# Kernel tuning notes

Measured on AMD Instinct MI355X. Metric: run time of the kernel, lower is better.

The kernel has to match this reference:

```python
import jax, jax.numpy as jnp
import numpy as np

B, T, D, H = 2, 2048, 1024, 16
HD = D // H  # 64


def _rotary_tables(t, hd):
    # standard RoPE cos/sin tables, shape [T, hd]
    inv_freq = 1.0 / (10000.0 ** (jnp.arange(0, hd, 2, dtype=jnp.float32) / hd))
    freqs = jnp.arange(t, dtype=jnp.float32)[:, None] * inv_freq[None, :]  # [T, hd/2]
    emb = jnp.concatenate([freqs, freqs], axis=-1)  # [T, hd]
    return jnp.cos(emb), jnp.sin(emb)


def setup_inputs() -> dict:
    key = jax.random.key(0)
    kx, kq, kk, kv, kp = jax.random.split(key, 5)
    x = jax.random.normal(kx, (B, T, D), dtype=jnp.float32)
    cos_t, sin_t = _rotary_tables(T, HD)
    cos = jnp.broadcast_to(cos_t[None], (B, T, HD)).astype(jnp.float32)
    sin = jnp.broadcast_to(sin_t[None], (B, T, HD)).astype(jnp.float32)
    scale = 0.02
    Wq = jax.random.normal(kq, (D, D), dtype=jnp.float32) * scale
    Wk = jax.random.normal(kk, (D, D), dtype=jnp.float32) * scale
    Wv = jax.random.normal(kv, (D, D), dtype=jnp.float32) * scale
    Wp = jax.random.normal(kp, (D, D), dtype=jnp.float32) * scale
    return {"x": x, "cos": cos, "sin": sin, "Wq": Wq, "Wk": Wk, "Wv": Wv, "Wp": Wp}


def _rotate_half(x):
    x1, x2 = jnp.split(x, 2, axis=-1)
    return jnp.concatenate([-x2, x1], axis=-1)


def reference(x, cos, sin, Wq, Wk, Wv, Wp):
    b, t, d = x.shape
    h, hd = H, HD
    # torch Linear: y = x @ W.T
    q = jnp.einsum('btd,ed->bte', x, Wq).reshape(b, t, h, hd)
    k = jnp.einsum('btd,ed->bte', x, Wk).reshape(b, t, h, hd)
    v = jnp.einsum('btd,ed->bte', x, Wv).reshape(b, t, h, hd)
    # RoPE, cos/sin [B,T,hd] -> broadcast over heads (unsqueeze_dim=2)
    c = cos[:, :, None, :]
    s = sin[:, :, None, :]
    q = q * c + _rotate_half(q) * s
    k = k * c + _rotate_half(k) * s
    # causal attention, softmax scale = 1/sqrt(head_dim) (flash_attn default)
    scale = 1.0 / np.sqrt(hd).astype(np.float32)
    scores = jnp.einsum('bqhd,bkhd->bhqk', q, k) * scale  # [B,H,T,T]
    mask = jnp.tril(jnp.ones((t, t), dtype=bool))
    scores = jnp.where(mask[None, None], scores, jnp.finfo(scores.dtype).min)
    probs = jax.nn.softmax(scores, axis=-1)
    out = jnp.einsum('bhqk,bkhd->bqhd', probs, v).reshape(b, t, d)
    return jnp.einsum('btd,ed->bte', out, Wp)
```

## Files before the change

### kernel.cpp

```cpp
#include <hip/hip_runtime.h>
#include <hip/hip_bf16.h>

typedef __attribute__((ext_vector_type(8))) short bf16x8s;
typedef __attribute__((ext_vector_type(4))) float f32x4;
typedef __attribute__((ext_vector_type(16))) float f32x16;
typedef __attribute__((ext_vector_type(4))) __bf16 bf16x4;
typedef __attribute__((ext_vector_type(8))) __bf16 bf16x8;

typedef const __attribute__((address_space(1))) void gvoid_t;
typedef __attribute__((address_space(3))) void lvoid_t;

constexpr int Bc = 2, Tc = 2048, Dc = 1024, Hc = 16, HDc = 64;
constexpr int Mc = Bc * Tc;

__global__ void cvt_all(const float* __restrict__ x,
                        const float* __restrict__ wq, const float* __restrict__ wk,
                        const float* __restrict__ wv, const float* __restrict__ wp,
                        __bf16* __restrict__ xb, __bf16* __restrict__ wb) {
  const int bid = blockIdx.x;
  const float* src;
  __bf16* dst;
  int i;
  if (bid < 4096) {
    src = x; dst = xb; i = (bid * 256 + threadIdx.x) * 4;
  } else {
    const int r = bid - 4096;
    const int w = r >> 10;
    src = (w == 0) ? wq : (w == 1) ? wk : (w == 2) ? wv : wp;
    dst = wb + (size_t)w * (Dc * Dc);
    i = ((r & 1023) * 256 + threadIdx.x) * 4;
  }
  float4 v = *(const float4*)(src + i);
  bf16x4 o;
  o[0] = (__bf16)v.x; o[1] = (__bf16)v.y; o[2] = (__bf16)v.z; o[3] = (__bf16)v.w;
  *(bf16x4*)(dst + i) = o;
}

__launch_bounds__(512, 2)
__global__ void gemm_qkv(const __bf16* __restrict__ A,
                         const __bf16* __restrict__ W,
                         __bf16* __restrict__ outb,
                         __bf16* __restrict__ vtout,
                         const float* __restrict__ cbt,
                         const float* __restrict__ sbt) {
  __shared__ __bf16 Albuf[2][128 * 64];
  __shared__ __bf16 Bbuf[2][3][128 * 64];
  const int tid = threadIdx.x;
  const int lane = tid & 63, wid = tid >> 6;
  const int wr = wid >> 1, wc = wid & 1;
  const int lr = lane & 15, lg = lane >> 4;
  const int lid = blockIdx.x + 8 * blockIdx.y;
  const int xcd = lid & 7, g = lid >> 3;
  const int brow = (xcd * 4 + (g & 3)) * 128;
  const int bcol = (g >> 2) * 128;

  f32x4 acc[3][2][4] = {};

  const char* Ag = (const char*)(A + (size_t)brow * Dc);
  const char* Bg = (const char*)(W + (size_t)bcol * Dc);
  const int r0s = tid >> 3;
  const int scol = (((tid & 7) ^ (r0s & 7)) << 4);
  const int lr7 = lr & 7;

#define STAGE(K0, BUF)                                                                    \
  do {                                                                                    \
    _Pragma("unroll")                                                                     \
    for (int i_ = 0; i_ < 2; ++i_) {                                                      \
      __builtin_amdgcn_global_load_lds(                                                   \
          (gvoid_t*)(Ag + (size_t)(i_ * 64 + r0s) * (Dc * 2) + (K0)*2 + scol),            \
          (lvoid_t*)((char*)Albuf[BUF] + i_ * 8192 + wid * 1024), 16, 0, 0);              \
      _Pragma("unroll")                                                                   \
      for (int z_ = 0; z_ < 3; ++z_)                                                      \
        __builtin_amdgcn_global_load_lds(                                                 \
            (gvoid_t*)(Bg + (size_t)z_ * (Dc * Dc * 2) +                                  \
                       (size_t)(i_ * 64 + r0s) * (Dc * 2) + (K0)*2 + scol),               \
            (lvoid_t*)((char*)Bbuf[BUF][z_] + i_ * 8192 + wid * 1024), 16, 0, 0);         \
    }                                                                                     \
  } while (0)

  STAGE(0, 0);
  asm volatile("s_waitcnt vmcnt(0)" ::: "memory");
  __builtin_amdgcn_sched_barrier(0);
  __builtin_amdgcn_s_barrier();
  __builtin_amdgcn_sched_barrier(0);

  for (int s = 0; s < 16; ++s) {
    if (s + 1 < 16) STAGE((s + 1) * 64, (s + 1) & 1);
    __builtin_amdgcn_sched_barrier(0);
    const char* Al = (const char*)Albuf[s & 1];
    const char* Bl0 = (const char*)Bbuf[s & 1][0];
#pragma unroll
    for (int kk = 0; kk < 2; ++kk) {
      const int sw = ((kk * 4 + lg) ^ lr7) << 4;
      bf16x8s af[2];
#pragma unroll
      for (int m = 0; m < 2; ++m)
        af[m] = *(const bf16x8s*)(Al + (wr * 32 + m * 16 + lr) * 128 + sw);
#pragma unroll
      for (int z = 0; z < 3; ++z) {
        const char* Bl = Bl0 + z * (128 * 64 * 2);
        bf16x8s bfv[4];
#pragma unroll
        for (int n = 0; n < 4; ++n)
          bfv[n] = *(const bf16x8s*)(Bl + (wc * 64 + n * 16 + lr) * 128 + sw);
        __builtin_amdgcn_s_setprio(1);
#pragma unroll
        for (int m = 0; m < 2; ++m)
#pragma unroll
          for (int n = 0; n < 4; ++n)
            acc[z][m][n] =
                __builtin_amdgcn_mfma_f32_16x16x32_bf16(af[m], bfv[n], acc[z][m][n], 0, 0, 0);
        __builtin_amdgcn_s_setprio(0);
      }
    }
    asm volatile("s_waitcnt vmcnt(0)" ::: "memory");
    __builtin_amdgcn_sched_barrier(0);
    __builtin_amdgcn_s_barrier();
    __builtin_amdgcn_sched_barrier(0);
  }
#undef STAGE

  const int h = (bcol >> 6) + wc;
#pragma unroll
  for (int z = 0; z < 2; ++z) {
    const float scl = (z == 0) ? 0.18033688011112042f : 1.0f;
    __bf16* dst = outb + (size_t)z * ((size_t)Mc * Dc);
#pragma unroll
    for (int m = 0; m < 2; ++m) {
#pragma unroll
      for (int j = 0; j < 4; ++j) {
        const int gm = brow + wr * 32 + m * 16 + lg * 4 + j;
        const int bb = gm >> 11, t = gm & (Tc - 1);
        const float* cbase = cbt + (size_t)gm * HDc;
        const float* sbase = sbt + (size_t)gm * HDc;
#pragma unroll
        for (int n = 0; n < 2; ++n) {
          const int i = n * 16 + lr;
          const float c0 = cbase[i], s0 = sbase[i];
          const float v0 = acc[z][m][n][j], v1 = acc[z][m][n + 2][j];
          acc[z][m][n][j]     = (v0 * c0 - v1 * s0) * scl;
          acc[z][m][n + 2][j] = (v1 * c0 + v0 * s0) * scl;
        }
        __bf16* rowp = dst + (((size_t)bb * Hc + h) * Tc + t) * HDc;
#pragma unroll
        for (int n = 0; n < 4; ++n) rowp[n * 16 + lr] = (__bf16)acc[z][m][n][j];
      }
    }
  }

  {
    const int bb2 = brow >> 11, t0b = brow & (Tc - 1);
    __bf16* tile_t = (__bf16*)Albuf;
#pragma unroll
    for (int h2 = 0; h2 < 2; ++h2) {
      __syncthreads();
      if (wc == h2) {
#pragma unroll
        for (int n = 0; n < 4; ++n)
#pragma unroll
          for (int m = 0; m < 2; ++m)
#pragma unroll
            for (int j = 0; j < 4; ++j)
              tile_t[(n * 16 + lr) * 136 + wr * 32 + m * 16 + lg * 4 + j] =
                  (__bf16)acc[2][m][n][j];
      }
      __syncthreads();
      const int hh2 = (bcol >> 6) + h2;
#pragma unroll
      for (int p = 0; p < 2; ++p) {
        const int r = p * 32 + (tid >> 4);
        const int c8 = (tid & 15) * 8;
        bf16x8 vvv = *(const bf16x8*)(tile_t + r * 136 + c8);
        *(bf16x8*)(vtout + (((size_t)bb2 * Hc + hh2) * HDc + r) * Tc + t0b + c8) = vvv;
      }
    }
  }
}

__launch_bounds__(256, 2)
__global__ void gemm_proj(const __bf16* __restrict__ A, const __bf16* __restrict__ W,
                          float* __restrict__ outf) {
  __shared__ __bf16 Alds[128 * 64];
  __shared__ __bf16 Blds[64 * 64];
  const int tid = threadIdx.x;
  const int lane = tid & 63, wid = tid >> 6;
  const int lr = lane & 15, lg = lane >> 4;
  const int lid = blockIdx.x + (int)gridDim.x * blockIdx.y;
  const int xcd = lid & 7, g = lid >> 3;
  const int brow = (xcd * 4 + (g & 3)) * 128;
  const int bcol = (g >> 2) * 64;
  f32x4 acc[2][4] = {};
  const char* Ag = (const char*)(A + (size_t)brow * Dc);
  const char* Bg = (const char*)(W + (size_t)bcol * Dc);
  const int r0 = tid >> 3;
  const int cb = (tid & 7) * 16;
  for (int k0 = 0; k0 < Dc; k0 += 64) {
#pragma unroll
    for (int i = 0; i < 4; ++i) {
      const int r = i * 32 + r0;
      const int ldsoff = (i * 256 + wid * 64) * 16;
      __builtin_amdgcn_global_load_lds(
          (gvoid_t*)(Ag + (size_t)r * (Dc * 2) + k0 * 2 + cb),
          (lvoid_t*)((char*)Alds + ldsoff), 16, 0, 0);
    }
#pragma unroll
    for (int i = 0; i < 2; ++i) {
      const int r = i * 32 + r0;
      const int ldsoff = (i * 256 + wid * 64) * 16;
      __builtin_amdgcn_global_load_lds(
          (gvoid_t*)(Bg + (size_t)r * (Dc * 2) + k0 * 2 + cb),
          (lvoid_t*)((char*)Blds + ldsoff), 16, 0, 0);
    }
    __syncthreads();
#pragma unroll
    for (int kk = 0; kk < 2; ++kk) {
      const int col = kk * 32 + lg * 8;
      bf16x8s af[2], bfv[4];
#pragma unroll
      for (int m = 0; m < 2; ++m)
        af[m] = *(const bf16x8s*)(Alds + (wid * 32 + m * 16 + lr) * 64 + col);
#pragma unroll
      for (int n = 0; n < 4; ++n)
        bfv[n] = *(const bf16x8s*)(Blds + (n * 16 + lr) * 64 + col);
#pragma unroll
      for (int m = 0; m < 2; ++m)
#pragma unroll
        for (int n = 0; n < 4; ++n)
          acc[m][n] = __builtin_amdgcn_mfma_f32_16x16x32_bf16(bfv[n], af[m], acc[m][n], 0, 0, 0);
    }
    __syncthreads();
  }
#pragma unroll
  for (int m = 0; m < 2; ++m) {
    const int gm = brow + wid * 32 + m * 16 + lr;
    float* rowp = outf + (size_t)gm * Dc + bcol;
#pragma unroll
    for (int n = 0; n < 4; ++n) {
      float4 fv;
      fv.x = acc[m][n][0]; fv.y = acc[m][n][1]; fv.z = acc[m][n][2]; fv.w = acc[m][n][3];
      *(float4*)(rowp + n * 16 + lg * 4) = fv;
    }
  }
}

__launch_bounds__(512, 4)
__global__ void attn_kernel(const __bf16* __restrict__ Q, const __bf16* __restrict__ K,
                            const __bf16* __restrict__ Vt, __bf16* __restrict__ O) {
  __shared__ __bf16 Klds[2][128 * 64];
  __shared__ __bf16 Vlds[2][64 * 128];
  const int f = blockIdx.x;
  const int xcd = f & 7, g = f >> 3;
  const int pass = g >> 4, g4 = g & 15;
  const int bh = xcd * 4 + pass;
  const int qt = ((pass >> 1) & 1) ? (15 - g4) : g4;
  const int tid = threadIdx.x;
  const int lane = tid & 63, wid = tid >> 6;
  const int qq = wid >> 1, kp = wid & 1;
  const int q31 = lane & 31, hh = lane >> 5;
  const int k3 = q31 & 7;
  const int v15 = q31 & 15;
  const __bf16* Qp = Q + (size_t)bh * Tc * HDc;
  const char* Kb = (const char*)(K + (size_t)bh * Tc * HDc);
  const char* Vb = (const char*)(Vt + (size_t)bh * HDc * Tc);

  const int units = qt + 1;

  const int sr = tid >> 3;
  const int sxor = ((tid & 7) ^ (sr & 7)) << 4;
  const int vr = tid >> 4;
  const int vxor = ((tid & 15) ^ (vr & 15)) << 4;
  const char* vsrc = Vb + (size_t)vr * (Tc * 2) + vxor;

  const int q0w = qt * 128 + qq * 32;
  bf16x8s qf[4];
#pragma unroll
  for (int ks = 0; ks < 4; ++ks)
    qf[ks] = *(const bf16x8s*)(Qp + (q0w + q31) * HDc + ks * 16 + hh * 8);

  const int b = bh >> 4, h = bh & 15;

  f32x16 acc0 = {}, acc1 = {};
  float lsum = 0.f;

#define STAGE(IT, BUF)                                                                   \
  do {                                                                                   \
    _Pragma("unroll")                                                                    \
    for (int i_ = 0; i_ < 2; ++i_) {                                                     \
      __builtin_amdgcn_global_load_lds(                                                  \
          (gvoid_t*)(Kb + (size_t)((IT) * 128 + i_ * 64 + sr) * 128 + sxor),             \
          (lvoid_t*)((char*)Klds[BUF] + i_ * 8192 + wid * 1024), 16, 0, 0);              \
      __builtin_amdgcn_global_load_lds(                                                  \
          (gvoid_t*)(vsrc + (size_t)i_ * 32 * (Tc * 2) + (IT) * 256),                    \
          (lvoid_t*)((char*)Vlds[BUF] + i_ * 8192 + wid * 1024), 16, 0, 0);              \
    }                                                                                    \
  } while (0)

  STAGE(0, 0);
  asm volatile("s_waitcnt vmcnt(0)" ::: "memory");
  __builtin_amdgcn_sched_barrier(0);
  __builtin_amdgcn_s_barrier();
  __builtin_amdgcn_sched_barrier(0);

  for (int u = 0; u < units; ++u) {
    if (u + 1 < units) STAGE(u + 1, (u + 1) & 1);
    __builtin_amdgcn_sched_barrier(0);

    const bool last = (u == qt);
    if (!(last && kp == 1 && qq < 2)) {
      const char* Kl = (const char*)Klds[u & 1];
      const char* Vl = (const char*)Vlds[u & 1];
      const bool fin = last && ((qq >> 1) == kp);
      const int thr = q0w + q31 - u * 128 - kp * 64 - 4 * hh;

#pragma unroll
      for (int ct = 0; ct < 2; ++ct) {
        bf16x8s kf[4];
#pragma unroll
        for (int ks = 0; ks < 4; ++ks)
          kf[ks] = *(const bf16x8s*)(Kl + (kp * 64 + ct * 32 + q31) * 128 +
                                     (((2 * ks + hh) ^ k3) << 4));
        f32x16 z = {};
        __builtin_amdgcn_s_setprio(1);
#pragma unroll
        for (int ks = 0; ks < 4; ++ks)
          z = __builtin_amdgcn_mfma_f32_32x32x16_bf16(kf[ks], qf[ks], z, 0, 0, 0);
        __builtin_amdgcn_s_setprio(0);

        unsigned w0[4], w1[4];
#pragma unroll
        for (int n = 0; n < 4; ++n) {
          float e[4];
#pragma unroll
          for (int j = 0; j < 4; ++j) {
            float ev = __builtin_amdgcn_exp2f(z[n * 4 + j]);
            if (fin && (ct * 32 + n * 8 + j > thr)) ev = 0.f;
            lsum += ev;
            e[j] = ev;
          }
          asm("v_cvt_pk_bf16_f32 %0, %1, %2" : "=v"(w0[n]) : "v"(e[0]), "v"(e[1]));
          asm("v_cvt_pk_bf16_f32 %0, %1, %2" : "=v"(w1[n]) : "v"(e[2]), "v"(e[3]));
        }

        bf16x8s pfr[2];
#pragma unroll
        for (int ks2 = 0; ks2 < 2; ++ks2) {
          unsigned a = w0[2 * ks2], bb2 = w0[2 * ks2 + 1];
          unsigned c = w1[2 * ks2], d = w1[2 * ks2 + 1];
          asm volatile("v_permlane32_swap_b32 %0, %1" : "+v"(a), "+v"(bb2));
          asm volatile("v_permlane32_swap_b32 %0, %1" : "+v"(c), "+v"(d));
          union { unsigned u[4]; bf16x8s v; } uu;
          uu.u[0] = a; uu.u[1] = c; uu.u[2] = bb2; uu.u[3] = d;
          pfr[ks2] = uu.v;
        }

        __builtin_amdgcn_s_setprio(1);
#pragma unroll
        for (int ks2 = 0; ks2 < 2; ++ks2) {
          const int so = ((kp * 8 + ct * 4 + 2 * ks2 + hh) ^ v15) << 4;
          const bf16x8s va0 = *(const bf16x8s*)(Vl + q31 * 256 + so);
          const bf16x8s va1 = *(const bf16x8s*)(Vl + (32 + q31) * 256 + so);
          acc0 = __builtin_amdgcn_mfma_f32_32x32x16_bf16(va0, pfr[ks2], acc0, 0, 0, 0);
          acc1 = __builtin_amdgcn_mfma_f32_32x32x16_bf16(va1, pfr[ks2], acc1, 0, 0, 0);
        }
        __builtin_amdgcn_s_setprio(0);
      }
    }

    if (u + 1 < units) {
      asm volatile("s_waitcnt vmcnt(0)" ::: "memory");
      __builtin_amdgcn_sched_barrier(0);
      __builtin_amdgcn_s_barrier();
      __builtin_amdgcn_sched_barrier(0);
    }
  }
#undef STAGE

  __syncthreads();
  float* kscr = (float*)&Klds[0][0];
  float* lscr = (float*)&Vlds[0][0];
  if (kp == 1) {
#pragma unroll
    for (int i = 0; i < 16; ++i) {
      kscr[qq * 2048 + i * 64 + lane] = acc0[i];
      kscr[qq * 2048 + 1024 + i * 64 + lane] = acc1[i];
    }
    lscr[qq * 64 + lane] = lsum;
  }
  __syncthreads();
  if (kp == 0) {
#pragma unroll
    for (int i = 0; i < 16; ++i) {
      acc0[i] += kscr[qq * 2048 + i * 64 + lane];
      acc1[i] += kscr[qq * 2048 + 1024 + i * 64 + lane];
    }
    lsum += lscr[qq * 64 + lane];
    const float lt = lsum + __shfl_xor(lsum, 32);
    const float linv = 1.f / lt;
    const int t = q0w + q31;
    __bf16* dst = O + ((size_t)b * Tc + t) * Dc + h * HDc;
#pragma unroll
    for (int qd = 0; qd < 4; ++qd) {
      bf16x4 o0, o1;
#pragma unroll
      for (int j = 0; j < 4; ++j) {
        o0[j] = (__bf16)(acc0[qd * 4 + j] * linv);
        o1[j] = (__bf16)(acc1[qd * 4 + j] * linv);
      }
      *(bf16x4*)(dst + qd * 8 + hh * 4) = o0;
      *(bf16x4*)(dst + 32 + qd * 8 + hh * 4) = o1;
    }
  }
}

extern "C" void kernel_launch(void* const* d_in, const int* in_sizes, int n_in,
                              void* d_out, int out_size, void* d_ws, size_t ws_size,
                              hipStream_t stream) {
  const float* x   = (const float*)d_in[0];
  const float* cbt = (const float*)d_in[1];
  const float* sbt = (const float*)d_in[2];
  const float* Wq  = (const float*)d_in[3];
  const float* Wk  = (const float*)d_in[4];
  const float* Wv  = (const float*)d_in[5];
  const float* Wp  = (const float*)d_in[6];
  float* out = (float*)d_out;
  char* ws = (char*)d_ws;
  __bf16* xb = (__bf16*)(ws);
  __bf16* wb = (__bf16*)(ws + (8u << 20));
  __bf16* qb = (__bf16*)(ws + (16u << 20));
  __bf16* vt = (__bf16*)(ws + (40u << 20));
  __bf16* ao = (__bf16*)(ws + (48u << 20));
  __bf16* kb = qb + (size_t)Mc * Dc;

  cvt_all<<<8192, 256, 0, stream>>>(x, Wq, Wk, Wv, Wp, xb, wb);
  gemm_qkv<<<dim3(8, 32), 512, 0, stream>>>(xb, wb, qb, vt, cbt, sbt);
  attn_kernel<<<512, 512, 0, stream>>>(qb, kb, vt, ao);
  gemm_proj<<<dim3(16, 32), 256, 0, stream>>>(ao, wb + 3u * (Dc * Dc), out);
}
```

Measured before the change: 95.52 us.

## Switch QKV GEMM to 4-stage K=32 pipeline with partial vmcnt waits

The QKV projection GEMM moves from a double-buffered K=64 loop to a four-buffer K=32 ring with two stages in flight, waiting only on the older loads via vmcnt counts instead of draining all loads each iteration. The LDS layout changes to pack two 32-wide rows per 128-byte line with a new XOR swizzle, and the fragment load addressing is updated to match. This is meant to hide global load latency better. In exchange it doubles the number of barriers and iterations, and the staging math must stay consistent with the swizzle.

```diff
diff --git a/kernel.cpp b/kernel.cpp
--- a/kernel.cpp
+++ b/kernel.cpp
@@ -43,8 +43,8 @@
                          __bf16* __restrict__ vtout,
                          const float* __restrict__ cbt,
                          const float* __restrict__ sbt) {
-  __shared__ __bf16 Albuf[2][128 * 64];
-  __shared__ __bf16 Bbuf[2][3][128 * 64];
+  __shared__ __bf16 Abuf[4][128 * 32];
+  __shared__ __bf16 Bbuf[4][3][128 * 32];
   const int tid = threadIdx.x;
   const int lane = tid & 63, wid = tid >> 6;
   const int wr = wid >> 1, wc = wid & 1;
@@ -58,65 +58,65 @@
 
   const char* Ag = (const char*)(A + (size_t)brow * Dc);
   const char* Bg = (const char*)(W + (size_t)bcol * Dc);
-  const int r0s = tid >> 3;
-  const int scol = (((tid & 7) ^ (r0s & 7)) << 4);
-  const int lr7 = lr & 7;
+  const int rp = tid >> 3;
+  const int unswz = (tid & 7) ^ (rp & 7);
+  const int srow = 2 * rp + (unswz >> 2);
+  const int skoff = (unswz & 3) * 16;
 
 #define STAGE(K0, BUF)                                                                    \
   do {                                                                                    \
+    __builtin_amdgcn_global_load_lds(                                                     \
+        (gvoid_t*)(Ag + (size_t)srow * (Dc * 2) + (K0)*2 + skoff),                        \
+        (lvoid_t*)((char*)Abuf[BUF] + tid * 16), 16, 0, 0);                               \
     _Pragma("unroll")                                                                     \
-    for (int i_ = 0; i_ < 2; ++i_) {                                                      \
+    for (int z_ = 0; z_ < 3; ++z_)                                                        \
       __builtin_amdgcn_global_load_lds(                                                   \
-          (gvoid_t*)(Ag + (size_t)(i_ * 64 + r0s) * (Dc * 2) + (K0)*2 + scol),            \
-          (lvoid_t*)((char*)Albuf[BUF] + i_ * 8192 + wid * 1024), 16, 0, 0);              \
-      _Pragma("unroll")                                                                   \
-      for (int z_ = 0; z_ < 3; ++z_)                                                      \
-        __builtin_amdgcn_global_load_lds(                                                 \
-            (gvoid_t*)(Bg + (size_t)z_ * (Dc * Dc * 2) +                                  \
-                       (size_t)(i_ * 64 + r0s) * (Dc * 2) + (K0)*2 + scol),               \
-            (lvoid_t*)((char*)Bbuf[BUF][z_] + i_ * 8192 + wid * 1024), 16, 0, 0);         \
-    }                                                                                     \
+          (gvoid_t*)(Bg + (size_t)z_ * (Dc * Dc * 2) + (size_t)srow * (Dc * 2) +          \
+                     (K0)*2 + skoff),                                                     \
+          (lvoid_t*)((char*)Bbuf[BUF][z_] + tid * 16), 16, 0, 0);                         \
   } while (0)
 
   STAGE(0, 0);
-  asm volatile("s_waitcnt vmcnt(0)" ::: "memory");
-  __builtin_amdgcn_sched_barrier(0);
-  __builtin_amdgcn_s_barrier();
-  __builtin_amdgcn_sched_barrier(0);
-
-  for (int s = 0; s < 16; ++s) {
-    if (s + 1 < 16) STAGE((s + 1) * 64, (s + 1) & 1);
-    __builtin_amdgcn_sched_barrier(0);
-    const char* Al = (const char*)Albuf[s & 1];
-    const char* Bl0 = (const char*)Bbuf[s & 1][0];
-#pragma unroll
-    for (int kk = 0; kk < 2; ++kk) {
-      const int sw = ((kk * 4 + lg) ^ lr7) << 4;
-      bf16x8s af[2];
-#pragma unroll
-      for (int m = 0; m < 2; ++m)
-        af[m] = *(const bf16x8s*)(Al + (wr * 32 + m * 16 + lr) * 128 + sw);
-#pragma unroll
-      for (int z = 0; z < 3; ++z) {
-        const char* Bl = Bl0 + z * (128 * 64 * 2);
-        bf16x8s bfv[4];
-#pragma unroll
-        for (int n = 0; n < 4; ++n)
-          bfv[n] = *(const bf16x8s*)(Bl + (wc * 64 + n * 16 + lr) * 128 + sw);
-        __builtin_amdgcn_s_setprio(1);
-#pragma unroll
-        for (int m = 0; m < 2; ++m)
-#pragma unroll
-          for (int n = 0; n < 4; ++n)
-            acc[z][m][n] =
-                __builtin_amdgcn_mfma_f32_16x16x32_bf16(af[m], bfv[n], acc[z][m][n], 0, 0, 0);
-        __builtin_amdgcn_s_setprio(0);
-      }
-    }
-    asm volatile("s_waitcnt vmcnt(0)" ::: "memory");
+  STAGE(32, 1);
+
+  const int swb = ((((lr & 1) << 2) | lg) ^ (lr >> 1)) << 4;
+  const int lrh = lr >> 1;
+
+  for (int s = 0; s < 32; ++s) {
+    if (s + 2 < 32) {
+      STAGE((s + 2) * 32, (s + 2) & 3);
+      asm volatile("s_waitcnt vmcnt(8)" ::: "memory");
+    } else if (s + 1 < 32) {
+      asm volatile("s_waitcnt vmcnt(4)" ::: "memory");
+    } else {
+      asm volatile("s_waitcnt vmcnt(0)" ::: "memory");
+    }
     __builtin_amdgcn_sched_barrier(0);
     __builtin_amdgcn_s_barrier();
     __builtin_amdgcn_sched_barrier(0);
+
+    const char* Al = (const char*)Abuf[s & 3];
+    const char* Bl0 = (const char*)Bbuf[s & 3][0];
+    bf16x8s af[2];
+#pragma unroll
+    for (int m = 0; m < 2; ++m)
+      af[m] = *(const bf16x8s*)(Al + (wr * 16 + m * 8 + lrh) * 128 + swb);
+#pragma unroll
+    for (int z = 0; z < 3; ++z) {
+      const char* Bl = Bl0 + z * (128 * 32 * 2);
+      bf16x8s bfv[4];
+#pragma unroll
+      for (int n = 0; n < 4; ++n)
+        bfv[n] = *(const bf16x8s*)(Bl + (wc * 32 + n * 8 + lrh) * 128 + swb);
+      __builtin_amdgcn_s_setprio(1);
+#pragma unroll
+      for (int m = 0; m < 2; ++m)
+#pragma unroll
+        for (int n = 0; n < 4; ++n)
+          acc[z][m][n] =
+              __builtin_amdgcn_mfma_f32_16x16x32_bf16(af[m], bfv[n], acc[z][m][n], 0, 0, 0);
+      __builtin_amdgcn_s_setprio(0);
+    }
   }
 #undef STAGE
 
@@ -150,7 +150,7 @@
 
   {
     const int bb2 = brow >> 11, t0b = brow & (Tc - 1);
-    __bf16* tile_t = (__bf16*)Albuf;
+    __bf16* tile_t = (__bf16*)Abuf;
 #pragma unroll
     for (int h2 = 0; h2 < 2; ++h2) {
       __syncthreads();
```

Result: faster. 92.98 us, median of 2 (-2.7%).
